# Kernel tuning notes

Measured on AMD Instinct MI355X. Metric: run time of the kernel, lower is better.

Reference implementation:

```python
import jax, jax.numpy as jnp
import numpy as np

N_EMBD = 1024
HEAD_SIZE = 64
B, T = 16, 2048


def setup_inputs() -> dict:
    key = jax.random.key(0)
    ks = jax.random.split(key, 7)
    s = 1.0 / np.sqrt(N_EMBD)
    return {
        "x": jax.random.normal(ks[0], (B, T, N_EMBD), dtype=jnp.float32),
        "Wq": jax.random.uniform(ks[1], (N_EMBD, HEAD_SIZE), jnp.float32, -s, s),
        "bq": jax.random.uniform(ks[2], (HEAD_SIZE,), jnp.float32, -s, s),
        "Wk": jax.random.uniform(ks[3], (N_EMBD, HEAD_SIZE), jnp.float32, -s, s),
        "bk": jax.random.uniform(ks[4], (HEAD_SIZE,), jnp.float32, -s, s),
        "Wv": jax.random.uniform(ks[5], (N_EMBD, HEAD_SIZE), jnp.float32, -s, s),
        "bv": jax.random.uniform(ks[6], (HEAD_SIZE,), jnp.float32, -s, s),
    }


def reference(x, Wq, bq, Wk, bk, Wv, bv):
    # x: [B, T, C]
    q = x @ Wq + bq          # [B, T, H]
    k = x @ Wk + bk          # [B, T, H]
    v = x @ Wv + bv          # [B, T, H]
    scale = k.shape[-1] ** -0.5
    wei = jnp.einsum("bth,bsh->bts", q, k) * scale  # [B, T, T]
    Tn = x.shape[1]
    causal = jnp.tril(jnp.ones((Tn, Tn), dtype=bool))
    wei = jnp.where(causal, wei, -jnp.inf)
    wei = jax.nn.softmax(wei, axis=-1)
    # dropout is identity in eval mode
    return jnp.einsum("bts,bsh->bth", wei, v)  # [B, T, H]
```

## Files before the change

kernel.cpp:

```cpp
#include <hip/hip_runtime.h>
#include <math.h>

#define BB 16
#define TT 2048
#define CC 1024
#define HH 64
#define MTOT (BB*TT)

typedef _Float16 f16;
typedef _Float16 f16x8 __attribute__((ext_vector_type(8)));
typedef float f32x4 __attribute__((ext_vector_type(4)));

#define WT_OFF 0
#define Q_OFF  196608
#define K_OFF  (Q_OFF + (size_t)MTOT*HH)
#define VT_OFF (K_OFF + (size_t)MTOT*HH)

__device__ __forceinline__ void async16(const void* g, void* l) {
    __builtin_amdgcn_global_load_lds(
        (const __attribute__((address_space(1))) unsigned int*)g,
        (__attribute__((address_space(3))) unsigned int*)l, 16, 0, 0);
}

__device__ __forceinline__ f16x8 cvt8(float4 u, float4 v) {
    f16x8 r;
    r[0] = (f16)u.x; r[1] = (f16)u.y; r[2] = (f16)u.z; r[3] = (f16)u.w;
    r[4] = (f16)v.x; r[5] = (f16)v.y; r[6] = (f16)v.z; r[7] = (f16)v.w;
    return r;
}

__global__ __launch_bounds__(256) void prep_kernel(
    const float* __restrict__ Wq, const float* __restrict__ Wk,
    const float* __restrict__ Wv, f16* __restrict__ ws)
{
    __shared__ f16 Ls[64][72];
    const int which = blockIdx.x >> 4, k0 = (blockIdx.x & 15) * 64;
    const float* W = (which == 0) ? Wq : (which == 1) ? Wk : Wv;
    const int t = threadIdx.x;
    const int kr = t >> 2, cb = t & 3;
    #pragma unroll
    for (int i = 0; i < 4; ++i) {
        float4 v = *(const float4*)(W + (size_t)(k0 + kr) * HH + cb * 16 + i * 4);
        Ls[kr][cb * 16 + i * 4 + 0] = (f16)v.x;
        Ls[kr][cb * 16 + i * 4 + 1] = (f16)v.y;
        Ls[kr][cb * 16 + i * 4 + 2] = (f16)v.z;
        Ls[kr][cb * 16 + i * 4 + 3] = (f16)v.w;
    }
    __syncthreads();
    const int n = t >> 2, kc = (t & 3) * 16;
    f16x8 o0, o1;
    #pragma unroll
    for (int i = 0; i < 8; ++i) o0[i] = Ls[kc + i][n];
    #pragma unroll
    for (int i = 0; i < 8; ++i) o1[i] = Ls[kc + 8 + i][n];
    f16* dst = ws + WT_OFF + (size_t)(which * 64 + n) * CC + k0 + kc;
    *(f16x8*)dst = o0;
    *(f16x8*)(dst + 8) = o1;
}

__global__ __launch_bounds__(256, 2) void qkv_kernel(
    const float* __restrict__ x,
    const float* __restrict__ bq, const float* __restrict__ bk,
    const float* __restrict__ bv, f16* __restrict__ ws)
{
    __shared__ __align__(16) float Xs[64 * 64];
    __shared__ __align__(16) f16   Ws[192 * 64];
    __shared__ __align__(16) f16   Vt[64][72];

    const f16* wt = ws + WT_OFF;
    const int tid  = threadIdx.x;
    const int lane = tid & 63, w = tid >> 6;
    const int c = lane & 15, g = lane >> 4;
    const int m0 = blockIdx.x * 64;

    f32x4 acc[4][3];
    #pragma unroll
    for (int mt = 0; mt < 4; ++mt)
        #pragma unroll
        for (int j = 0; j < 3; ++j) acc[mt][j] = (f32x4){0.f, 0.f, 0.f, 0.f};

    for (int k0 = 0; k0 < CC; k0 += 64) {
        __syncthreads();
        #pragma unroll
        for (int i = 0; i < 4; ++i) {
            int G0 = (w * 4 + i) * 64;
            int G = G0 + lane;
            int r = G >> 4, q = G & 15;
            async16(x + (size_t)(m0 + r) * CC + k0 + ((q ^ (r & 15)) << 2),
                    Xs + G0 * 4);
        }
        #pragma unroll
        for (int i = 0; i < 6; ++i) {
            int G0 = (w * 6 + i) * 64;
            int G = G0 + lane;
            int r = G >> 3, q = G & 7;
            async16(wt + (size_t)r * CC + k0 + ((q ^ (r & 7)) << 3),
                    Ws + G0 * 8);
        }
        __syncthreads();

        #pragma unroll
        for (int kk = 0; kk < 2; ++kk) {
            f16x8 bfr[3];
            #pragma unroll
            for (int j = 0; j < 3; ++j) {
                int r = (3 * w + j) * 16 + c;
                int p = (kk * 4 + g) ^ (c & 7);
                bfr[j] = *(const f16x8*)(Ws + r * 64 + p * 8);
            }
            #pragma unroll
            for (int mt = 0; mt < 4; ++mt) {
                int r = mt * 16 + c;
                int q = kk * 8 + 2 * g;
                float4 f0 = *(const float4*)(Xs + r * 64 + (q ^ c) * 4);
                float4 f1 = *(const float4*)(Xs + r * 64 + ((q + 1) ^ c) * 4);
                f16x8 a = cvt8(f0, f1);
                #pragma unroll
                for (int j = 0; j < 3; ++j)
                    acc[mt][j] = __builtin_amdgcn_mfma_f32_16x16x32_f16(
                        a, bfr[j], acc[mt][j], 0, 0, 0);
            }
        }
    }

    const float QSCALE = 0.125f * 1.44269504089f;
    #pragma unroll
    for (int j = 0; j < 3; ++j) {
        int nt = 3 * w + j;
        int plane = nt >> 2;
        int h = (nt & 3) * 16 + c;
        if (plane == 0) {
            float bias = bq[h];
            #pragma unroll
            for (int mt = 0; mt < 4; ++mt)
                #pragma unroll
                for (int r = 0; r < 4; ++r) {
                    int m = m0 + mt * 16 + 4 * g + r;
                    ws[Q_OFF + (size_t)m * HH + h] =
                        (f16)((acc[mt][j][r] + bias) * QSCALE);
                }
        } else if (plane == 1) {
            float bias = bk[h];
            #pragma unroll
            for (int mt = 0; mt < 4; ++mt)
                #pragma unroll
                for (int r = 0; r < 4; ++r) {
                    int m = m0 + mt * 16 + 4 * g + r;
                    ws[K_OFF + (size_t)m * HH + h] = (f16)(acc[mt][j][r] + bias);
                }
        } else {
            float bias = bv[h];
            #pragma unroll
            for (int mt = 0; mt < 4; ++mt)
                #pragma unroll
                for (int r = 0; r < 4; ++r)
                    Vt[h][mt * 16 + 4 * g + r] = (f16)(acc[mt][j][r] + bias);
        }
    }
    __syncthreads();
    {
        int h = tid >> 2, seg = tid & 3;
        f16* dst = ws + VT_OFF + (size_t)h * MTOT + m0 + seg * 16;
        *(f16x8*)dst       = *(f16x8*)&Vt[h][seg * 16];
        *(f16x8*)(dst + 8) = *(f16x8*)&Vt[h][seg * 16 + 8];
    }
}

__global__ __launch_bounds__(128, 3) void attn_kernel(
    const f16* __restrict__ ws, float* __restrict__ out)
{
    const f16* qp = ws + Q_OFF;
    const f16* kp = ws + K_OFF;
    const f16* vt = ws + VT_OFF;

    __shared__ __align__(16) f16 Ks[64 * 64];
    __shared__ __align__(16) f16 Vs[64 * 64];
    __shared__ __align__(16) f16 Ps[2][16][72];

    const int tid  = threadIdx.x;
    const int lane = tid & 63, w = tid >> 6;
    const int c = lane & 15, g = lane >> 4;

    const int id = blockIdx.x;
    const int r8 = id & 7, j = id >> 3;
    const int half = j >> 6, qr = j & 63;
    const int b  = 2 * r8 + half;
    const int qi = half ? (63 - qr) : qr;
    const int q0 = qi * 32;
    const int stmax = qi >> 1;
    const size_t rowbase = (size_t)b * TT;

    const f16* qrow = qp + (rowbase + q0 + w * 16 + c) * HH;
    const f16x8 aq0 = *(const f16x8*)(qrow + 8 * g);
    const f16x8 aq1 = *(const f16x8*)(qrow + 32 + 8 * g);

    f32x4 o[5];
    #pragma unroll
    for (int nt = 0; nt < 5; ++nt) o[nt] = (f32x4){0.f, 0.f, 0.f, 0.f};

    f16x8 onesf;
    #pragma unroll
    for (int i = 0; i < 8; ++i) onesf[i] = (c == 0) ? (f16)1.0f : (f16)0.0f;

    for (int st = 0; st <= stmax; ++st) {
        const int s0 = st * 64;
        __syncthreads();
        #pragma unroll
        for (int i = 0; i < 4; ++i) {
            int G0 = (w * 4 + i) * 64;
            int G = G0 + lane;
            int r = G >> 3, q = G & 7;
            int sw = (q ^ (r & 7)) << 3;
            async16(kp + (rowbase + s0 + r) * HH + sw, Ks + G0 * 8);
            async16(vt + (size_t)r * MTOT + rowbase + s0 + sw, Vs + G0 * 8);
        }
        __syncthreads();

        f32x4 s[4];
        #pragma unroll
        for (int nt = 0; nt < 4; ++nt) {
            s[nt] = (f32x4){0.f, 0.f, 0.f, 0.f};
            int r = nt * 16 + c;
            f16x8 b0 = *(const f16x8*)(Ks + r * 64 + ((g       ^ (c & 7)) << 3));
            f16x8 b1 = *(const f16x8*)(Ks + r * 64 + (((4 + g) ^ (c & 7)) << 3));
            s[nt] = __builtin_amdgcn_mfma_f32_16x16x32_f16(aq0, b0, s[nt], 0, 0, 0);
            s[nt] = __builtin_amdgcn_mfma_f32_16x16x32_f16(aq1, b1, s[nt], 0, 0, 0);
        }

        if (st == stmax) {
            const int doff = q0 - s0;
            #pragma unroll
            for (int nt = 0; nt < 4; ++nt)
                #pragma unroll
                for (int rr = 0; rr < 4; ++rr)
                    if (nt * 16 + c > doff + w * 16 + 4 * g + rr)
                        s[nt][rr] = -INFINITY;
        }

        #pragma unroll
        for (int nt = 0; nt < 4; ++nt)
            #pragma unroll
            for (int rr = 0; rr < 4; ++rr)
                Ps[w][4 * g + rr][nt * 16 + c] = (f16)__builtin_exp2f(s[nt][rr]);
        f16x8 pa0 = *(f16x8*)&Ps[w][c][g * 8];
        f16x8 pa1 = *(f16x8*)&Ps[w][c][32 + g * 8];

        #pragma unroll
        for (int nt = 0; nt < 4; ++nt) {
            int r = nt * 16 + c;
            f16x8 v0 = *(const f16x8*)(Vs + r * 64 + ((g       ^ (c & 7)) << 3));
            f16x8 v1 = *(const f16x8*)(Vs + r * 64 + (((4 + g) ^ (c & 7)) << 3));
            o[nt] = __builtin_amdgcn_mfma_f32_16x16x32_f16(pa0, v0, o[nt], 0, 0, 0);
            o[nt] = __builtin_amdgcn_mfma_f32_16x16x32_f16(pa1, v1, o[nt], 0, 0, 0);
        }
        o[4] = __builtin_amdgcn_mfma_f32_16x16x32_f16(pa0, onesf, o[4], 0, 0, 0);
        o[4] = __builtin_amdgcn_mfma_f32_16x16x32_f16(pa1, onesf, o[4], 0, 0, 0);
    }

    #pragma unroll
    for (int rr = 0; rr < 4; ++rr) {
        float lv = __shfl(o[4][rr], lane & 48);
        float inv = 1.0f / lv;
        int mrow = q0 + w * 16 + 4 * g + rr;
        #pragma unroll
        for (int nt = 0; nt < 4; ++nt)
            out[(rowbase + mrow) * HH + nt * 16 + c] = o[nt][rr] * inv;
    }
}

extern "C" void kernel_launch(void* const* d_in, const int* in_sizes, int n_in,
                              void* d_out, int out_size, void* d_ws, size_t ws_size,
                              hipStream_t stream) {
    const float* x  = (const float*)d_in[0];
    const float* Wq = (const float*)d_in[1];
    const float* bq = (const float*)d_in[2];
    const float* Wk = (const float*)d_in[3];
    const float* bk = (const float*)d_in[4];
    const float* Wv = (const float*)d_in[5];
    const float* bv = (const float*)d_in[6];
    f16*   ws  = (f16*)d_ws;
    float* out = (float*)d_out;

    prep_kernel<<<48, 256, 0, stream>>>(Wq, Wk, Wv, ws);
    qkv_kernel<<<MTOT / 64, 256, 0, stream>>>(x, bq, bk, bv, ws);
    attn_kernel<<<1024, 128, 0, stream>>>(ws, out);
}
```

Measured before the change: 248.3 us.

## Split causal KV range across warp pairs and read K/V directly from global

The attention kernel now uses four warps per block, with two warp pairs each processing half of the key/value tiles for the same 32 queries. Partial outputs and row sums are combined through shared memory before normalisation. K and V fragments are loaded straight from global memory instead of being staged through LDS, which removes per-tile barriers but relies on cache hits. The QKV projection kernel uses 32-row tiles with higher occupancy to get more blocks in flight.

```diff
diff --git a/kernel.cpp b/kernel.cpp
--- a/kernel.cpp
+++ b/kernel.cpp
@@ -58,32 +58,32 @@
     *(f16x8*)(dst + 8) = o1;
 }
 
-__global__ __launch_bounds__(256, 2) void qkv_kernel(
+__global__ __launch_bounds__(256, 4) void qkv_kernel(
     const float* __restrict__ x,
     const float* __restrict__ bq, const float* __restrict__ bk,
     const float* __restrict__ bv, f16* __restrict__ ws)
 {
-    __shared__ __align__(16) float Xs[64 * 64];
+    __shared__ __align__(16) float Xs[32 * 64];
     __shared__ __align__(16) f16   Ws[192 * 64];
-    __shared__ __align__(16) f16   Vt[64][72];
+    __shared__ __align__(16) f16   Vt[64][36];
 
     const f16* wt = ws + WT_OFF;
     const int tid  = threadIdx.x;
     const int lane = tid & 63, w = tid >> 6;
     const int c = lane & 15, g = lane >> 4;
-    const int m0 = blockIdx.x * 64;
-
-    f32x4 acc[4][3];
-    #pragma unroll
-    for (int mt = 0; mt < 4; ++mt)
+    const int m0 = blockIdx.x * 32;
+
+    f32x4 acc[2][3];
+    #pragma unroll
+    for (int mt = 0; mt < 2; ++mt)
         #pragma unroll
         for (int j = 0; j < 3; ++j) acc[mt][j] = (f32x4){0.f, 0.f, 0.f, 0.f};
 
     for (int k0 = 0; k0 < CC; k0 += 64) {
         __syncthreads();
         #pragma unroll
-        for (int i = 0; i < 4; ++i) {
-            int G0 = (w * 4 + i) * 64;
+        for (int i = 0; i < 2; ++i) {
+            int G0 = (w * 2 + i) * 64;
             int G = G0 + lane;
             int r = G >> 4, q = G & 15;
             async16(x + (size_t)(m0 + r) * CC + k0 + ((q ^ (r & 15)) << 2),
@@ -109,7 +109,7 @@
                 bfr[j] = *(const f16x8*)(Ws + r * 64 + p * 8);
             }
             #pragma unroll
-            for (int mt = 0; mt < 4; ++mt) {
+            for (int mt = 0; mt < 2; ++mt) {
                 int r = mt * 16 + c;
                 int q = kk * 8 + 2 * g;
                 float4 f0 = *(const float4*)(Xs + r * 64 + (q ^ c) * 4);
@@ -132,7 +132,7 @@
         if (plane == 0) {
             float bias = bq[h];
             #pragma unroll
-            for (int mt = 0; mt < 4; ++mt)
+            for (int mt = 0; mt < 2; ++mt)
                 #pragma unroll
                 for (int r = 0; r < 4; ++r) {
                     int m = m0 + mt * 16 + 4 * g + r;
@@ -142,7 +142,7 @@
         } else if (plane == 1) {
             float bias = bk[h];
             #pragma unroll
-            for (int mt = 0; mt < 4; ++mt)
+            for (int mt = 0; mt < 2; ++mt)
                 #pragma unroll
                 for (int r = 0; r < 4; ++r) {
                     int m = m0 + mt * 16 + 4 * g + r;
@@ -151,35 +151,35 @@
         } else {
             float bias = bv[h];
             #pragma unroll
-            for (int mt = 0; mt < 4; ++mt)
+            for (int mt = 0; mt < 2; ++mt)
                 #pragma unroll
                 for (int r = 0; r < 4; ++r)
                     Vt[h][mt * 16 + 4 * g + r] = (f16)(acc[mt][j][r] + bias);
         }
     }
     __syncthreads();
-    {
-        int h = tid >> 2, seg = tid & 3;
+    if (tid < 128) {
+        int h = tid >> 1, seg = tid & 1;
         f16* dst = ws + VT_OFF + (size_t)h * MTOT + m0 + seg * 16;
         *(f16x8*)dst       = *(f16x8*)&Vt[h][seg * 16];
         *(f16x8*)(dst + 8) = *(f16x8*)&Vt[h][seg * 16 + 8];
     }
 }
 
-__global__ __launch_bounds__(128, 3) void attn_kernel(
+__global__ __launch_bounds__(256, 4) void attn_kernel(
     const f16* __restrict__ ws, float* __restrict__ out)
 {
     const f16* qp = ws + Q_OFF;
     const f16* kp = ws + K_OFF;
     const f16* vt = ws + VT_OFF;
 
-    __shared__ __align__(16) f16 Ks[64 * 64];
-    __shared__ __align__(16) f16 Vs[64 * 64];
-    __shared__ __align__(16) f16 Ps[2][16][72];
+    __shared__ __align__(16) f16 Ps[4][16][72];
+    __shared__ __align__(16) float Ob[2][16][65];
 
     const int tid  = threadIdx.x;
     const int lane = tid & 63, w = tid >> 6;
     const int c = lane & 15, g = lane >> 4;
+    const int wq = w & 1, pair = w >> 1;
 
     const int id = blockIdx.x;
     const int r8 = id & 7, j = id >> 3;
@@ -187,10 +187,13 @@
     const int b  = 2 * r8 + half;
     const int qi = half ? (63 - qr) : qr;
     const int q0 = qi * 32;
-    const int stmax = qi >> 1;
+    const int nst = (qi >> 1) + 1;
+    const int nsplit = (nst + 1) >> 1;
+    const int st_lo = pair ? nsplit : 0;
+    const int st_hi = pair ? nst : nsplit;
     const size_t rowbase = (size_t)b * TT;
 
-    const f16* qrow = qp + (rowbase + q0 + w * 16 + c) * HH;
+    const f16* qrow = qp + (rowbase + q0 + wq * 16 + c) * HH;
     const f16x8 aq0 = *(const f16x8*)(qrow + 8 * g);
     const f16x8 aq1 = *(const f16x8*)(qrow + 32 + 8 * g);
 
@@ -202,38 +205,26 @@
     #pragma unroll
     for (int i = 0; i < 8; ++i) onesf[i] = (c == 0) ? (f16)1.0f : (f16)0.0f;
 
-    for (int st = 0; st <= stmax; ++st) {
+    for (int st = st_lo; st < st_hi; ++st) {
         const int s0 = st * 64;
-        __syncthreads();
-        #pragma unroll
-        for (int i = 0; i < 4; ++i) {
-            int G0 = (w * 4 + i) * 64;
-            int G = G0 + lane;
-            int r = G >> 3, q = G & 7;
-            int sw = (q ^ (r & 7)) << 3;
-            async16(kp + (rowbase + s0 + r) * HH + sw, Ks + G0 * 8);
-            async16(vt + (size_t)r * MTOT + rowbase + s0 + sw, Vs + G0 * 8);
-        }
-        __syncthreads();
 
         f32x4 s[4];
         #pragma unroll
         for (int nt = 0; nt < 4; ++nt) {
             s[nt] = (f32x4){0.f, 0.f, 0.f, 0.f};
-            int r = nt * 16 + c;
-            f16x8 b0 = *(const f16x8*)(Ks + r * 64 + ((g       ^ (c & 7)) << 3));
-            f16x8 b1 = *(const f16x8*)(Ks + r * 64 + (((4 + g) ^ (c & 7)) << 3));
+            const f16* krow = kp + (rowbase + s0 + nt * 16 + c) * HH;
+            f16x8 b0 = *(const f16x8*)(krow + 8 * g);
+            f16x8 b1 = *(const f16x8*)(krow + 32 + 8 * g);
             s[nt] = __builtin_amdgcn_mfma_f32_16x16x32_f16(aq0, b0, s[nt], 0, 0, 0);
             s[nt] = __builtin_amdgcn_mfma_f32_16x16x32_f16(aq1, b1, s[nt], 0, 0, 0);
         }
 
-        if (st == stmax) {
-            const int doff = q0 - s0;
+        if (st == nst - 1) {
             #pragma unroll
             for (int nt = 0; nt < 4; ++nt)
                 #pragma unroll
                 for (int rr = 0; rr < 4; ++rr)
-                    if (nt * 16 + c > doff + w * 16 + 4 * g + rr)
+                    if (s0 + nt * 16 + c > q0 + wq * 16 + 4 * g + rr)
                         s[nt][rr] = -INFINITY;
         }
 
@@ -247,9 +238,9 @@
 
         #pragma unroll
         for (int nt = 0; nt < 4; ++nt) {
-            int r = nt * 16 + c;
-            f16x8 v0 = *(const f16x8*)(Vs + r * 64 + ((g       ^ (c & 7)) << 3));
-            f16x8 v1 = *(const f16x8*)(Vs + r * 64 + (((4 + g) ^ (c & 7)) << 3));
+            const f16* vrow = vt + (size_t)(nt * 16 + c) * MTOT + rowbase + s0;
+            f16x8 v0 = *(const f16x8*)(vrow + 8 * g);
+            f16x8 v1 = *(const f16x8*)(vrow + 32 + 8 * g);
             o[nt] = __builtin_amdgcn_mfma_f32_16x16x32_f16(pa0, v0, o[nt], 0, 0, 0);
             o[nt] = __builtin_amdgcn_mfma_f32_16x16x32_f16(pa1, v1, o[nt], 0, 0, 0);
         }
@@ -257,14 +248,38 @@
         o[4] = __builtin_amdgcn_mfma_f32_16x16x32_f16(pa1, onesf, o[4], 0, 0, 0);
     }
 
-    #pragma unroll
-    for (int rr = 0; rr < 4; ++rr) {
-        float lv = __shfl(o[4][rr], lane & 48);
-        float inv = 1.0f / lv;
-        int mrow = q0 + w * 16 + 4 * g + rr;
+    if (pair == 1) {
         #pragma unroll
         for (int nt = 0; nt < 4; ++nt)
-            out[(rowbase + mrow) * HH + nt * 16 + c] = o[nt][rr] * inv;
+            #pragma unroll
+            for (int rr = 0; rr < 4; ++rr)
+                Ob[wq][4 * g + rr][nt * 16 + c] = o[nt][rr];
+        if (c == 0) {
+            #pragma unroll
+            for (int rr = 0; rr < 4; ++rr)
+                Ob[wq][4 * g + rr][64] = o[4][rr];
+        }
+    }
+    __syncthreads();
+    if (pair == 0) {
+        #pragma unroll
+        for (int nt = 0; nt < 4; ++nt)
+            #pragma unroll
+            for (int rr = 0; rr < 4; ++rr)
+                o[nt][rr] += Ob[wq][4 * g + rr][nt * 16 + c];
+        #pragma unroll
+        for (int rr = 0; rr < 4; ++rr)
+            o[4][rr] += Ob[wq][4 * g + rr][64];
+
+        #pragma unroll
+        for (int rr = 0; rr < 4; ++rr) {
+            float lv = __shfl(o[4][rr], lane & 48);
+            float inv = 1.0f / lv;
+            int mrow = q0 + wq * 16 + 4 * g + rr;
+            #pragma unroll
+            for (int nt = 0; nt < 4; ++nt)
+                out[(rowbase + mrow) * HH + nt * 16 + c] = o[nt][rr] * inv;
+        }
     }
 }
 
@@ -282,6 +297,6 @@
     float* out = (float*)d_out;
 
     prep_kernel<<<48, 256, 0, stream>>>(Wq, Wk, Wv, ws);
-    qkv_kernel<<<MTOT / 64, 256, 0, stream>>>(x, bq, bk, bv, ws);
-    attn_kernel<<<1024, 128, 0, stream>>>(ws, out);
-}
+    qkv_kernel<<<MTOT / 32, 256, 0, stream>>>(x, bq, bk, bv, ws);
+    attn_kernel<<<1024, 256, 0, stream>>>(ws, out);
+}
```

Result: slower. 278.6 us (+12.2%).
